# Optimization experiments

Measured on AMD Instinct MI355X. Metric: run time of the kernel, lower is better.

The kernel has to match this reference:

```python
import math
import jax, jax.numpy as jnp
import numpy as np

NUM_HEADS = 8


def setup_inputs() -> dict:
    rng = jax.random.key(0)
    ks = jax.random.split(rng, 6)
    S, B, E = 2048, 4, 512
    scale = 1.0 / math.sqrt(E)  # xavier-ish init scale
    return {
        "query": jax.random.normal(ks[0], (S, B, E), jnp.float32),
        "key": jax.random.normal(ks[1], (S, B, E), jnp.float32),
        "value": jax.random.normal(ks[2], (S, B, E), jnp.float32),
        "attn_mask": jax.random.normal(ks[3], (B, S, S), jnp.float32),
        "in_proj_weight": jax.random.normal(ks[4], (3 * E, E), jnp.float32) * scale,
        "in_proj_bias": jnp.zeros((3 * E,), jnp.float32),
        "out_proj_weight": jax.random.normal(ks[5], (E, E), jnp.float32) * scale,
        "out_proj_bias": jnp.zeros((E,), jnp.float32),
    }


def reference(query, key, value, attn_mask, in_proj_weight, in_proj_bias,
              out_proj_weight, out_proj_bias):
    # Layout: [S, B, E] (batch_first=False)
    S, B, E = query.shape
    H = NUM_HEADS
    D = E // H
    w_q, w_k, w_v = jnp.split(in_proj_weight, 3, axis=0)  # each [E, E]
    b_q, b_k, b_v = jnp.split(in_proj_bias, 3)
    q = query @ w_q.T + b_q
    k = key @ w_k.T + b_k
    v = value @ w_v.T + b_v

    def to_heads(x):  # [S,B,E] -> [B,H,S,D]
        return x.reshape(S, B, H, D).transpose(1, 2, 0, 3)

    qh = to_heads(q) * (1.0 / math.sqrt(D))
    kh = to_heads(k)
    vh = to_heads(v)
    # full score matrix [B,H,S,S] with per-batch additive mask broadcast over heads
    scores = jnp.einsum('bhsd,bhtd->bhst', qh, kh) + attn_mask[:, None, :, :]
    attn = jax.nn.softmax(scores, axis=-1)
    out = jnp.einsum('bhst,bhtd->bhsd', attn, vh)
    out = out.transpose(2, 0, 1, 3).reshape(S, B, E)  # back to [S,B,E]
    return out @ out_proj_weight.T + out_proj_bias
```

## Files before the change

kernel.cpp:

```cpp
#include <hip/hip_runtime.h>


#define L2E 1.44269504088896340736f

typedef __attribute__((ext_vector_type(8))) __bf16 bf16x8;
typedef __attribute__((ext_vector_type(4))) float f32x4;

static __device__ __forceinline__ unsigned short f2bf(float f) {
    union { float f; unsigned u; } v; v.f = f;
    unsigned u = v.u + 0x7fffu + ((v.u >> 16) & 1u);
    return (unsigned short)(u >> 16);
}

static __device__ __forceinline__ unsigned cvtpk(float a, float b) {
    unsigned r;
    asm("v_cvt_pk_bf16_f32 %0, %1, %2" : "=v"(r) : "v"(a), "v"(b));
    return r;
}

__global__ __launch_bounds__(256) void qkv_kernel(
    const float* __restrict__ Xq, const float* __restrict__ Xk,
    const float* __restrict__ Xv, const float* __restrict__ W,
    const float* __restrict__ bias,
    unsigned short* __restrict__ Qp, unsigned short* __restrict__ Kp,
    unsigned short* __restrict__ Vt)
{
    __shared__ unsigned short lA[128][40];
    __shared__ unsigned short lB[128][40];

    const int z = blockIdx.z;
    const float* X  = (z == 0) ? Xq : (z == 1) ? Xk : Xv;
    const float* Wz = W + (size_t)z * 512 * 512;
    const int rb = blockIdx.y * 128;
    const int nb = blockIdx.x * 128;
    const int tid  = threadIdx.x;
    const int lane = tid & 63, wave = tid >> 6;
    const int wr = wave >> 1, wc = wave & 1;
    const int lq = lane & 15, lg = lane >> 4;

    f32x4 acc[4][4];
#pragma unroll
    for (int i = 0; i < 4; ++i)
#pragma unroll
        for (int j = 0; j < 4; ++j) acc[i][j] = (f32x4){0.f, 0.f, 0.f, 0.f};

    const int srow = tid >> 1;
    const int scol = (tid & 1) * 16;

    for (int kt = 0; kt < 16; ++kt) {
        const int k0 = kt * 32;
        if (kt) __syncthreads();
        {
            const float* g = X + (size_t)(rb + srow) * 512 + k0 + scol;
            float4 x0 = *(const float4*)(g + 0);
            float4 x1 = *(const float4*)(g + 4);
            float4 x2 = *(const float4*)(g + 8);
            float4 x3 = *(const float4*)(g + 12);
            uint4 w0, w1;
            w0.x = cvtpk(x0.x, x0.y); w0.y = cvtpk(x0.z, x0.w);
            w0.z = cvtpk(x1.x, x1.y); w0.w = cvtpk(x1.z, x1.w);
            w1.x = cvtpk(x2.x, x2.y); w1.y = cvtpk(x2.z, x2.w);
            w1.z = cvtpk(x3.x, x3.y); w1.w = cvtpk(x3.z, x3.w);
            *(uint4*)&lA[srow][scol] = w0;
            *(uint4*)&lA[srow][scol + 8] = w1;
        }
        {
            const float* g = Wz + (size_t)(nb + srow) * 512 + k0 + scol;
            float4 x0 = *(const float4*)(g + 0);
            float4 x1 = *(const float4*)(g + 4);
            float4 x2 = *(const float4*)(g + 8);
            float4 x3 = *(const float4*)(g + 12);
            uint4 w0, w1;
            w0.x = cvtpk(x0.x, x0.y); w0.y = cvtpk(x0.z, x0.w);
            w0.z = cvtpk(x1.x, x1.y); w0.w = cvtpk(x1.z, x1.w);
            w1.x = cvtpk(x2.x, x2.y); w1.y = cvtpk(x2.z, x2.w);
            w1.z = cvtpk(x3.x, x3.y); w1.w = cvtpk(x3.z, x3.w);
            *(uint4*)&lB[srow][scol] = w0;
            *(uint4*)&lB[srow][scol + 8] = w1;
        }
        __syncthreads();

        bf16x8 af[4], bf[4];
#pragma unroll
        for (int mi = 0; mi < 4; ++mi)
            af[mi] = *(const bf16x8*)&lA[wr * 64 + mi * 16 + lq][lg * 8];
#pragma unroll
        for (int ni = 0; ni < 4; ++ni)
            bf[ni] = *(const bf16x8*)&lB[wc * 64 + ni * 16 + lq][lg * 8];
#pragma unroll
        for (int mi = 0; mi < 4; ++mi)
#pragma unroll
            for (int ni = 0; ni < 4; ++ni)
                acc[mi][ni] = __builtin_amdgcn_mfma_f32_16x16x32_bf16(
                    af[mi], bf[ni], acc[mi][ni], 0, 0, 0);
    }

    const float* bz = bias + z * 512;
#pragma unroll
    for (int ni = 0; ni < 4; ++ni) {
        const int n = nb + wc * 64 + ni * 16 + lq;
        const float bv = bz[n];
        const int h = n >> 6, d = n & 63;
#pragma unroll
        for (int mi = 0; mi < 4; ++mi) {
#pragma unroll
            for (int r = 0; r < 4; ++r) {
                const int t = rb + wr * 64 + mi * 16 + lg * 4 + r;
                float v = acc[mi][ni][r] + bv;
                const int s = t >> 2, b = t & 3;
                if (z == 0) {
                    v *= 0.125f;
                    Qp[((size_t)(b * 8 + h) * 2048 + s) * 64 + d] = f2bf(v);
                } else if (z == 1) {
                    Kp[((size_t)(b * 8 + h) * 2048 + s) * 64 + d] = f2bf(v);
                } else {
                    Vt[((size_t)(b * 8 + h) * 64 + d) * 2048 + s] = f2bf(v);
                }
            }
        }
    }
}

__global__ __launch_bounds__(256) void attn_kernel(
    const unsigned short* __restrict__ Qp, const unsigned short* __restrict__ Kp,
    const unsigned short* __restrict__ Vt, const float* __restrict__ mask,
    unsigned short* __restrict__ AO)
{
    __shared__ unsigned short lK[64][72];
    __shared__ unsigned short lV[64][72];
    __shared__ unsigned short lP[4][16][72];

    const int bh = blockIdx.y;
    const int b = bh >> 3, h = bh & 7;
    const int qb = blockIdx.x * 64;
    const int tid  = threadIdx.x;
    const int lane = tid & 63, wave = tid >> 6;
    const int lq = lane & 15, lg = lane >> 4;

    const int qloc = wave * 16 + lq;
    const int qg = qb + qloc;
    const unsigned short* Kbase = Kp + (size_t)bh * 2048 * 64;
    const unsigned short* Vbase = Vt + (size_t)bh * 64 * 2048;
    const float* mrow = mask + ((size_t)b * 2048 + qg) * 2048 + lg * 4;

    const bf16x8 qf0 = *(const bf16x8*)(Qp + ((size_t)bh * 2048 + qg) * 64 + lg * 8);
    const bf16x8 qf1 = *(const bf16x8*)(Qp + ((size_t)bh * 2048 + qg) * 64 + 32 + lg * 8);

    f32x4 o[4];
#pragma unroll
    for (int di = 0; di < 4; ++di) o[di] = (f32x4){0.f, 0.f, 0.f, 0.f};
    float m = -3.0e38f, l = 0.f;

    const int srow = tid >> 2;
    const int sseg = (tid & 3) * 16;

    for (int kb = 0; kb < 32; ++kb) {
        const int kv = kb * 64;
        if (kb) __syncthreads();
        {
            const unsigned short* g = Kbase + (size_t)(kv + srow) * 64 + sseg;
            *(uint4*)&lK[srow][sseg]     = *(const uint4*)g;
            *(uint4*)&lK[srow][sseg + 8] = *(const uint4*)(g + 8);
        }
        {
            const unsigned short* g = Vbase + (size_t)srow * 2048 + kv + sseg;
            *(uint4*)&lV[srow][sseg]     = *(const uint4*)g;
            *(uint4*)&lV[srow][sseg + 8] = *(const uint4*)(g + 8);
        }
        float4 mv[4];
#pragma unroll
        for (int sub = 0; sub < 4; ++sub)
            mv[sub] = *(const float4*)(mrow + kv + sub * 16);
        __syncthreads();

        f32x4 zv[4];
#pragma unroll
        for (int sub = 0; sub < 4; ++sub) {
            bf16x8 a0 = *(const bf16x8*)&lK[sub * 16 + lq][lg * 8];
            bf16x8 a1 = *(const bf16x8*)&lK[sub * 16 + lq][32 + lg * 8];
            f32x4 sf = (f32x4){mv[sub].x, mv[sub].y, mv[sub].z, mv[sub].w};
            sf = __builtin_amdgcn_mfma_f32_16x16x32_bf16(a0, qf0, sf, 0, 0, 0);
            sf = __builtin_amdgcn_mfma_f32_16x16x32_bf16(a1, qf1, sf, 0, 0, 0);
            zv[sub] = sf;
        }

        float mb = zv[0][0];
#pragma unroll
        for (int sub = 0; sub < 4; ++sub)
#pragma unroll
            for (int r = 0; r < 4; ++r) mb = fmaxf(mb, zv[sub][r]);
        mb = fmaxf(mb, __shfl_xor(mb, 16));
        mb = fmaxf(mb, __shfl_xor(mb, 32));

        if (!__all(mb <= m + 8.0f)) {
            const float mn = fmaxf(m, mb);
            const float al = exp2f((m - mn) * L2E);
#pragma unroll
            for (int di = 0; di < 4; ++di) {
                o[di][0] *= al; o[di][1] *= al; o[di][2] *= al; o[di][3] *= al;
            }
            l *= al;
            m = mn;
        }

        float ps = 0.f;
        unsigned pw[4][2];
#pragma unroll
        for (int sub = 0; sub < 4; ++sub) {
            float p0 = exp2f((zv[sub][0] - m) * L2E);
            float p1 = exp2f((zv[sub][1] - m) * L2E);
            float p2 = exp2f((zv[sub][2] - m) * L2E);
            float p3 = exp2f((zv[sub][3] - m) * L2E);
            ps += (p0 + p1) + (p2 + p3);
            pw[sub][0] = cvtpk(p0, p1);
            pw[sub][1] = cvtpk(p2, p3);
        }
        ps += __shfl_xor(ps, 16);
        ps += __shfl_xor(ps, 32);
        l += ps;

#pragma unroll
        for (int sub = 0; sub < 4; ++sub)
            *(uint2*)&lP[wave][lq][sub * 16 + lg * 4] = make_uint2(pw[sub][0], pw[sub][1]);

#pragma unroll
        for (int ks = 0; ks < 2; ++ks) {
            bf16x8 pb = *(const bf16x8*)&lP[wave][lq][ks * 32 + lg * 8];
#pragma unroll
            for (int di = 0; di < 4; ++di) {
                bf16x8 av = *(const bf16x8*)&lV[di * 16 + lq][ks * 32 + lg * 8];
                o[di] = __builtin_amdgcn_mfma_f32_16x16x32_bf16(av, pb, o[di], 0, 0, 0);
            }
        }
    }

    const float inv = 1.0f / l;
    unsigned short* aobase = AO + ((size_t)qg * 4 + b) * 512 + h * 64;
#pragma unroll
    for (int di = 0; di < 4; ++di) {
        const int d = di * 16 + lg * 4;
        unsigned u0 = cvtpk(o[di][0] * inv, o[di][1] * inv);
        unsigned u1 = cvtpk(o[di][2] * inv, o[di][3] * inv);
        *(uint2*)(aobase + d) = make_uint2(u0, u1);
    }
}

__global__ __launch_bounds__(256) void oproj_kernel(
    const unsigned short* __restrict__ A, const float* __restrict__ W,
    const float* __restrict__ bias, float* __restrict__ out)
{
    __shared__ unsigned short lA[128][40];
    __shared__ unsigned short lB[128][40];

    const int rb = blockIdx.y * 128;
    const int nb = blockIdx.x * 128;
    const int tid  = threadIdx.x;
    const int lane = tid & 63, wave = tid >> 6;
    const int wr = wave >> 1, wc = wave & 1;
    const int lq = lane & 15, lg = lane >> 4;

    f32x4 acc[4][4];
#pragma unroll
    for (int i = 0; i < 4; ++i)
#pragma unroll
        for (int j = 0; j < 4; ++j) acc[i][j] = (f32x4){0.f, 0.f, 0.f, 0.f};

    const int srow = tid >> 1;
    const int scol = (tid & 1) * 16;

    for (int kt = 0; kt < 16; ++kt) {
        const int k0 = kt * 32;
        if (kt) __syncthreads();
        {
            const unsigned short* g = A + (size_t)(rb + srow) * 512 + k0 + scol;
            *(uint4*)&lA[srow][scol]     = *(const uint4*)g;
            *(uint4*)&lA[srow][scol + 8] = *(const uint4*)(g + 8);
        }
        {
            const float* g = W + (size_t)(nb + srow) * 512 + k0 + scol;
            float4 x0 = *(const float4*)(g + 0);
            float4 x1 = *(const float4*)(g + 4);
            float4 x2 = *(const float4*)(g + 8);
            float4 x3 = *(const float4*)(g + 12);
            uint4 w0, w1;
            w0.x = cvtpk(x0.x, x0.y); w0.y = cvtpk(x0.z, x0.w);
            w0.z = cvtpk(x1.x, x1.y); w0.w = cvtpk(x1.z, x1.w);
            w1.x = cvtpk(x2.x, x2.y); w1.y = cvtpk(x2.z, x2.w);
            w1.z = cvtpk(x3.x, x3.y); w1.w = cvtpk(x3.z, x3.w);
            *(uint4*)&lB[srow][scol] = w0;
            *(uint4*)&lB[srow][scol + 8] = w1;
        }
        __syncthreads();

        bf16x8 af[4], bfr[4];
#pragma unroll
        for (int mi = 0; mi < 4; ++mi)
            af[mi] = *(const bf16x8*)&lA[wr * 64 + mi * 16 + lq][lg * 8];
#pragma unroll
        for (int ni = 0; ni < 4; ++ni)
            bfr[ni] = *(const bf16x8*)&lB[wc * 64 + ni * 16 + lq][lg * 8];
#pragma unroll
        for (int mi = 0; mi < 4; ++mi)
#pragma unroll
            for (int ni = 0; ni < 4; ++ni)
                acc[mi][ni] = __builtin_amdgcn_mfma_f32_16x16x32_bf16(
                    af[mi], bfr[ni], acc[mi][ni], 0, 0, 0);
    }

#pragma unroll
    for (int ni = 0; ni < 4; ++ni) {
        const int n = nb + wc * 64 + ni * 16 + lq;
        const float bv = bias[n];
#pragma unroll
        for (int mi = 0; mi < 4; ++mi) {
#pragma unroll
            for (int r = 0; r < 4; ++r) {
                const int t = rb + wr * 64 + mi * 16 + lg * 4 + r;
                out[(size_t)t * 512 + n] = acc[mi][ni][r] + bv;
            }
        }
    }
}

extern "C" void kernel_launch(void* const* d_in, const int* in_sizes, int n_in,
                              void* d_out, int out_size, void* d_ws, size_t ws_size,
                              hipStream_t stream)
{
    (void)in_sizes; (void)n_in; (void)out_size; (void)ws_size;
    const float* query = (const float*)d_in[0];
    const float* key   = (const float*)d_in[1];
    const float* value = (const float*)d_in[2];
    const float* mask  = (const float*)d_in[3];
    const float* w_in  = (const float*)d_in[4];
    const float* b_in  = (const float*)d_in[5];
    const float* w_out = (const float*)d_in[6];
    const float* b_out = (const float*)d_in[7];
    float* out = (float*)d_out;

    char* ws = (char*)d_ws;
    unsigned short* Qp = (unsigned short*)(ws);
    unsigned short* Kp = (unsigned short*)(ws + (size_t)8 * 1024 * 1024);
    unsigned short* Vt = (unsigned short*)(ws + (size_t)16 * 1024 * 1024);
    unsigned short* AO = (unsigned short*)(ws + (size_t)24 * 1024 * 1024);

    qkv_kernel<<<dim3(4, 64, 3), 256, 0, stream>>>(query, key, value, w_in, b_in,
                                                   Qp, Kp, Vt);
    attn_kernel<<<dim3(32, 32), 256, 0, stream>>>(Qp, Kp, Vt, mask, AO);
    oproj_kernel<<<dim3(4, 64), 256, 0, stream>>>(AO, w_out, b_out, out);
}
```

Baseline: 156.7 us.

## Double-buffer K/V tiles in attention and prefetch mask via registers

The attention kernel now keeps two LDS buffers for K and V. The next tile's K, V and mask values are loaded into registers while the current tile is computed, then written to the other buffer, which removes one barrier per iteration. MFMA sections are wrapped in s_setprio, and the inline-asm bf16 pack is replaced with compiler __bf16 casts. The change uses more LDS and registers, which may lower occupancy.

New measurement: 170.7 us. 1.09x slower.

```diff
diff --git a/kernel.cpp b/kernel.cpp
--- a/kernel.cpp
+++ b/kernel.cpp
@@ -6,16 +6,16 @@
 typedef __attribute__((ext_vector_type(8))) __bf16 bf16x8;
 typedef __attribute__((ext_vector_type(4))) float f32x4;
 
+static __device__ __forceinline__ unsigned pk2(float a, float b) {
+    union { unsigned u; __bf16 h[2]; } cv;
+    cv.h[0] = (__bf16)a; cv.h[1] = (__bf16)b;
+    return cv.u;
+}
+
 static __device__ __forceinline__ unsigned short f2bf(float f) {
-    union { float f; unsigned u; } v; v.f = f;
-    unsigned u = v.u + 0x7fffu + ((v.u >> 16) & 1u);
-    return (unsigned short)(u >> 16);
-}
-
-static __device__ __forceinline__ unsigned cvtpk(float a, float b) {
-    unsigned r;
-    asm("v_cvt_pk_bf16_f32 %0, %1, %2" : "=v"(r) : "v"(a), "v"(b));
-    return r;
+    union { unsigned short s; __bf16 h; } cv;
+    cv.h = (__bf16)f;
+    return cv.s;
 }
 
 __global__ __launch_bounds__(256) void qkv_kernel(
@@ -57,10 +57,10 @@
             float4 x2 = *(const float4*)(g + 8);
             float4 x3 = *(const float4*)(g + 12);
             uint4 w0, w1;
-            w0.x = cvtpk(x0.x, x0.y); w0.y = cvtpk(x0.z, x0.w);
-            w0.z = cvtpk(x1.x, x1.y); w0.w = cvtpk(x1.z, x1.w);
-            w1.x = cvtpk(x2.x, x2.y); w1.y = cvtpk(x2.z, x2.w);
-            w1.z = cvtpk(x3.x, x3.y); w1.w = cvtpk(x3.z, x3.w);
+            w0.x = pk2(x0.x, x0.y); w0.y = pk2(x0.z, x0.w);
+            w0.z = pk2(x1.x, x1.y); w0.w = pk2(x1.z, x1.w);
+            w1.x = pk2(x2.x, x2.y); w1.y = pk2(x2.z, x2.w);
+            w1.z = pk2(x3.x, x3.y); w1.w = pk2(x3.z, x3.w);
             *(uint4*)&lA[srow][scol] = w0;
             *(uint4*)&lA[srow][scol + 8] = w1;
         }
@@ -71,10 +71,10 @@
             float4 x2 = *(const float4*)(g + 8);
             float4 x3 = *(const float4*)(g + 12);
             uint4 w0, w1;
-            w0.x = cvtpk(x0.x, x0.y); w0.y = cvtpk(x0.z, x0.w);
-            w0.z = cvtpk(x1.x, x1.y); w0.w = cvtpk(x1.z, x1.w);
-            w1.x = cvtpk(x2.x, x2.y); w1.y = cvtpk(x2.z, x2.w);
-            w1.z = cvtpk(x3.x, x3.y); w1.w = cvtpk(x3.z, x3.w);
+            w0.x = pk2(x0.x, x0.y); w0.y = pk2(x0.z, x0.w);
+            w0.z = pk2(x1.x, x1.y); w0.w = pk2(x1.z, x1.w);
+            w1.x = pk2(x2.x, x2.y); w1.y = pk2(x2.z, x2.w);
+            w1.z = pk2(x3.x, x3.y); w1.w = pk2(x3.z, x3.w);
             *(uint4*)&lB[srow][scol] = w0;
             *(uint4*)&lB[srow][scol + 8] = w1;
         }
@@ -126,8 +126,8 @@
     const unsigned short* __restrict__ Vt, const float* __restrict__ mask,
     unsigned short* __restrict__ AO)
 {
-    __shared__ unsigned short lK[64][72];
-    __shared__ unsigned short lV[64][72];
+    __shared__ unsigned short lK[2][64][72];
+    __shared__ unsigned short lV[2][64][72];
     __shared__ unsigned short lP[4][16][72];
 
     const int bh = blockIdx.y;
@@ -137,8 +137,7 @@
     const int lane = tid & 63, wave = tid >> 6;
     const int lq = lane & 15, lg = lane >> 4;
 
-    const int qloc = wave * 16 + lq;
-    const int qg = qb + qloc;
+    const int qg = qb + wave * 16 + lq;
     const unsigned short* Kbase = Kp + (size_t)bh * 2048 * 64;
     const unsigned short* Vbase = Vt + (size_t)bh * 64 * 2048;
     const float* mrow = mask + ((size_t)b * 2048 + qg) * 2048 + lg * 4;
@@ -153,42 +152,55 @@
 
     const int srow = tid >> 2;
     const int sseg = (tid & 3) * 16;
+    const unsigned short* gK = Kbase + (size_t)srow * 64 + sseg;
+    const unsigned short* gV = Vbase + (size_t)srow * 2048 + sseg;
+
+    uint4 ka = *(const uint4*)(gK);
+    uint4 kc = *(const uint4*)(gK + 8);
+    uint4 va = *(const uint4*)(gV);
+    uint4 vc = *(const uint4*)(gV + 8);
+    float4 mv[4];
+#pragma unroll
+    for (int sub = 0; sub < 4; ++sub)
+        mv[sub] = *(const float4*)(mrow + sub * 16);
+    *(uint4*)&lK[0][srow][sseg]     = ka;
+    *(uint4*)&lK[0][srow][sseg + 8] = kc;
+    *(uint4*)&lV[0][srow][sseg]     = va;
+    *(uint4*)&lV[0][srow][sseg + 8] = vc;
+    __syncthreads();
 
     for (int kb = 0; kb < 32; ++kb) {
-        const int kv = kb * 64;
-        if (kb) __syncthreads();
-        {
-            const unsigned short* g = Kbase + (size_t)(kv + srow) * 64 + sseg;
-            *(uint4*)&lK[srow][sseg]     = *(const uint4*)g;
-            *(uint4*)&lK[srow][sseg + 8] = *(const uint4*)(g + 8);
-        }
-        {
-            const unsigned short* g = Vbase + (size_t)srow * 2048 + kv + sseg;
-            *(uint4*)&lV[srow][sseg]     = *(const uint4*)g;
-            *(uint4*)&lV[srow][sseg + 8] = *(const uint4*)(g + 8);
-        }
-        float4 mv[4];
-#pragma unroll
-        for (int sub = 0; sub < 4; ++sub)
-            mv[sub] = *(const float4*)(mrow + kv + sub * 16);
-        __syncthreads();
+        const int cur = kb & 1;
+        float4 mnx[4];
+        if (kb < 31) {
+            const size_t kv = (size_t)(kb + 1) * 64;
+            ka = *(const uint4*)(gK + kv * 64);
+            kc = *(const uint4*)(gK + kv * 64 + 8);
+            va = *(const uint4*)(gV + kv);
+            vc = *(const uint4*)(gV + kv + 8);
+#pragma unroll
+            for (int sub = 0; sub < 4; ++sub)
+                mnx[sub] = *(const float4*)(mrow + kv + sub * 16);
+        }
 
         f32x4 zv[4];
+        __builtin_amdgcn_s_setprio(1);
 #pragma unroll
         for (int sub = 0; sub < 4; ++sub) {
-            bf16x8 a0 = *(const bf16x8*)&lK[sub * 16 + lq][lg * 8];
-            bf16x8 a1 = *(const bf16x8*)&lK[sub * 16 + lq][32 + lg * 8];
+            bf16x8 a0 = *(const bf16x8*)&lK[cur][sub * 16 + lq][lg * 8];
+            bf16x8 a1 = *(const bf16x8*)&lK[cur][sub * 16 + lq][32 + lg * 8];
             f32x4 sf = (f32x4){mv[sub].x, mv[sub].y, mv[sub].z, mv[sub].w};
             sf = __builtin_amdgcn_mfma_f32_16x16x32_bf16(a0, qf0, sf, 0, 0, 0);
             sf = __builtin_amdgcn_mfma_f32_16x16x32_bf16(a1, qf1, sf, 0, 0, 0);
             zv[sub] = sf;
         }
-
-        float mb = zv[0][0];
-#pragma unroll
-        for (int sub = 0; sub < 4; ++sub)
-#pragma unroll
-            for (int r = 0; r < 4; ++r) mb = fmaxf(mb, zv[sub][r]);
+        __builtin_amdgcn_s_setprio(0);
+
+        float t0 = fmaxf(fmaxf(zv[0][0], zv[0][1]), fmaxf(zv[0][2], zv[0][3]));
+        float t1 = fmaxf(fmaxf(zv[1][0], zv[1][1]), fmaxf(zv[1][2], zv[1][3]));
+        float t2 = fmaxf(fmaxf(zv[2][0], zv[2][1]), fmaxf(zv[2][2], zv[2][3]));
+        float t3 = fmaxf(fmaxf(zv[3][0], zv[3][1]), fmaxf(zv[3][2], zv[3][3]));
+        float mb = fmaxf(fmaxf(t0, t1), fmaxf(t2, t3));
         mb = fmaxf(mb, __shfl_xor(mb, 16));
         mb = fmaxf(mb, __shfl_xor(mb, 32));
 
@@ -203,35 +215,50 @@
             m = mn;
         }
 
-        float ps = 0.f;
-        unsigned pw[4][2];
+        float p[16];
 #pragma unroll
         for (int sub = 0; sub < 4; ++sub) {
-            float p0 = exp2f((zv[sub][0] - m) * L2E);
-            float p1 = exp2f((zv[sub][1] - m) * L2E);
-            float p2 = exp2f((zv[sub][2] - m) * L2E);
-            float p3 = exp2f((zv[sub][3] - m) * L2E);
-            ps += (p0 + p1) + (p2 + p3);
-            pw[sub][0] = cvtpk(p0, p1);
-            pw[sub][1] = cvtpk(p2, p3);
-        }
+            p[sub * 4 + 0] = exp2f((zv[sub][0] - m) * L2E);
+            p[sub * 4 + 1] = exp2f((zv[sub][1] - m) * L2E);
+            p[sub * 4 + 2] = exp2f((zv[sub][2] - m) * L2E);
+            p[sub * 4 + 3] = exp2f((zv[sub][3] - m) * L2E);
+        }
+        float s0 = (p[0] + p[1]) + (p[2] + p[3]);
+        float s1 = (p[4] + p[5]) + (p[6] + p[7]);
+        float s2 = (p[8] + p[9]) + (p[10] + p[11]);
+        float s3 = (p[12] + p[13]) + (p[14] + p[15]);
+        float ps = (s0 + s1) + (s2 + s3);
         ps += __shfl_xor(ps, 16);
         ps += __shfl_xor(ps, 32);
         l += ps;
 
 #pragma unroll
         for (int sub = 0; sub < 4; ++sub)
-            *(uint2*)&lP[wave][lq][sub * 16 + lg * 4] = make_uint2(pw[sub][0], pw[sub][1]);
-
+            *(uint2*)&lP[wave][lq][sub * 16 + lg * 4] =
+                make_uint2(pk2(p[sub * 4 + 0], p[sub * 4 + 1]),
+                           pk2(p[sub * 4 + 2], p[sub * 4 + 3]));
+
+        __builtin_amdgcn_s_setprio(1);
 #pragma unroll
         for (int ks = 0; ks < 2; ++ks) {
             bf16x8 pb = *(const bf16x8*)&lP[wave][lq][ks * 32 + lg * 8];
 #pragma unroll
             for (int di = 0; di < 4; ++di) {
-                bf16x8 av = *(const bf16x8*)&lV[di * 16 + lq][ks * 32 + lg * 8];
+                bf16x8 av = *(const bf16x8*)&lV[cur][di * 16 + lq][ks * 32 + lg * 8];
                 o[di] = __builtin_amdgcn_mfma_f32_16x16x32_bf16(av, pb, o[di], 0, 0, 0);
             }
         }
+        __builtin_amdgcn_s_setprio(0);
+
+        if (kb < 31) {
+            *(uint4*)&lK[cur ^ 1][srow][sseg]     = ka;
+            *(uint4*)&lK[cur ^ 1][srow][sseg + 8] = kc;
+            *(uint4*)&lV[cur ^ 1][srow][sseg]     = va;
+            *(uint4*)&lV[cur ^ 1][srow][sseg + 8] = vc;
+#pragma unroll
+            for (int sub = 0; sub < 4; ++sub) mv[sub] = mnx[sub];
+        }
+        __syncthreads();
     }
 
     const float inv = 1.0f / l;
@@ -239,9 +266,8 @@
 #pragma unroll
     for (int di = 0; di < 4; ++di) {
         const int d = di * 16 + lg * 4;
-        unsigned u0 = cvtpk(o[di][0] * inv, o[di][1] * inv);
-        unsigned u1 = cvtpk(o[di][2] * inv, o[di][3] * inv);
-        *(uint2*)(aobase + d) = make_uint2(u0, u1);
+        *(uint2*)(aobase + d) = make_uint2(pk2(o[di][0] * inv, o[di][1] * inv),
+                                           pk2(o[di][2] * inv, o[di][3] * inv));
     }
 }
 
@@ -283,10 +309,10 @@
             float4 x2 = *(const float4*)(g + 8);
             float4 x3 = *(const float4*)(g + 12);
             uint4 w0, w1;
-            w0.x = cvtpk(x0.x, x0.y); w0.y = cvtpk(x0.z, x0.w);
-            w0.z = cvtpk(x1.x, x1.y); w0.w = cvtpk(x1.z, x1.w);
-            w1.x = cvtpk(x2.x, x2.y); w1.y = cvtpk(x2.z, x2.w);
-            w1.z = cvtpk(x3.x, x3.y); w1.w = cvtpk(x3.z, x3.w);
+            w0.x = pk2(x0.x, x0.y); w0.y = pk2(x0.z, x0.w);
+            w0.z = pk2(x1.x, x1.y); w0.w = pk2(x1.z, x1.w);
+            w1.x = pk2(x2.x, x2.y); w1.y = pk2(x2.z, x2.w);
+            w1.z = pk2(x3.x, x3.y); w1.w = pk2(x3.z, x3.w);
             *(uint4*)&lB[srow][scol] = w0;
             *(uint4*)&lB[srow][scol + 8] = w1;
         }
```
